# Kernel tuning notes

Measured on AMD Instinct MI355X. Metric: run time of the kernel, lower is better.

Reference implementation:

```python
import jax, jax.numpy as jnp
import numpy as np

N_NODES = 100000
N_EDGES = 1200000
D = 64  # in = hid = out = 64


def _seg_sum(vals, idx, n):
    return jax.ops.segment_sum(vals, idx, num_segments=n)


def _graph_conv(x, src, dst, W, b, n_nodes):
    # dgl.nn.GraphConv with norm='both', bias=True:
    #   h = (D_out^-1/2 applied to src feats) -> sum over edges -> D_in^-1/2 -> +b
    # Weight applied first (math-equivalent linear, in==out dims here).
    e = src.shape[0]
    ones = jnp.ones((e,), x.dtype)
    deg_out = jnp.clip(_seg_sum(ones, src, n_nodes), 1.0)  # zero-deg clamp, as in DGL
    deg_in = jnp.clip(_seg_sum(ones, dst, n_nodes), 1.0)
    h = (x @ W) * jax.lax.rsqrt(deg_out)[:, None]          # [N, D]
    agg = _seg_sum(h[src], dst, n_nodes)                   # gather-scatter over edges
    return agg * jax.lax.rsqrt(deg_in)[:, None] + b


def _rgcn(x, edges, params, n_nodes):
    # HeteroGraphConv(aggregate='sum'): sum per-relation GraphConv outputs.
    (s0, d0), (s1, d1) = edges
    h = (_graph_conv(x, s0, d0, params['W1_0'], params['b1_0'], n_nodes)
         + _graph_conv(x, s1, d1, params['W1_1'], params['b1_1'], n_nodes))
    h = jax.nn.relu(h)
    h = (_graph_conv(h, s0, d0, params['W2_0'], params['b2_0'], n_nodes)
         + _graph_conv(h, s1, d1, params['W2_1'], params['b2_1'], n_nodes))
    return h


def setup_inputs() -> dict:
    key = jax.random.key(0)
    ks = jax.random.split(key, 16)
    inp = {
        'x': jax.random.normal(ks[0], (N_NODES, D), dtype=jnp.float32),
        'rel0_src': jax.random.randint(ks[1], (N_EDGES,), 0, N_NODES, dtype=jnp.int32),
        'rel0_dst': jax.random.randint(ks[2], (N_EDGES,), 0, N_NODES, dtype=jnp.int32),
        'rel1_src': jax.random.randint(ks[3], (N_EDGES,), 0, N_NODES, dtype=jnp.int32),
        'rel1_dst': jax.random.randint(ks[4], (N_EDGES,), 0, N_NODES, dtype=jnp.int32),
        'neg_src': jax.random.randint(ks[5], (N_EDGES,), 0, N_NODES, dtype=jnp.int32),
        'neg_dst': jax.random.randint(ks[6], (N_EDGES,), 0, N_NODES, dtype=jnp.int32),
    }
    scale = 1.0 / np.sqrt(D)
    for i, name in enumerate(['W1_0', 'W1_1', 'W2_0', 'W2_1']):
        inp[name] = jax.random.normal(ks[7 + i], (D, D), dtype=jnp.float32) * scale
    for name in ['b1_0', 'b1_1', 'b2_0', 'b2_1']:
        inp[name] = jnp.zeros((D,), dtype=jnp.float32)
    return inp


def reference(x, rel0_src, rel0_dst, rel1_src, rel1_dst, neg_src, neg_dst,
              W1_0, W1_1, W2_0, W2_1, b1_0, b1_1, b2_0, b2_1):
    params = {'W1_0': W1_0, 'b1_0': b1_0, 'W1_1': W1_1, 'b1_1': b1_1,
              'W2_0': W2_0, 'b2_0': b2_0, 'W2_1': W2_1, 'b2_1': b2_1}
    edges = ((rel0_src, rel0_dst), (rel1_src, rel1_dst))
    h = _rgcn(x, edges, params, N_NODES)  # [N, D]
    # HeteroDotProductPredictor: u_dot_v on etype edges -> [E, 1]
    pos_score = jnp.sum(h[rel0_src] * h[rel0_dst], axis=-1, keepdims=True)
    neg_score = jnp.sum(h[neg_src] * h[neg_dst], axis=-1, keepdims=True)
    return pos_score, neg_score
```

## Files before the change

kernel.cpp:

```cpp
#include <hip/hip_runtime.h>
#include <hip/hip_fp16.h>

#define N_NODES 100000
#define N_EDGES 1200000
#define TOTAL_E (2 * N_EDGES)
#define D 64

#define BSH 7
#define NBUCK 782
#define NCHUNK 320
#define CHUNK 7500
#define HIST_L (NBUCK * NCHUNK)
#define SCAN_BS 256
#define SCAN_NB ((HIST_L + SCAN_BS - 1) / SCAN_BS)
#define ENT_CAP 4608
#define L2M_GRID ((N_NODES + 127) / 128)
#define NKEY 2048

typedef __attribute__((ext_vector_type(8))) short bf16x8;
typedef __attribute__((ext_vector_type(4))) float f32x4;

__device__ __forceinline__ unsigned short f32_bf16_rne(float f) {
    unsigned u = __float_as_uint(f);
    unsigned r = u + 0x7FFF + ((u >> 16) & 1);
    return (unsigned short)(r >> 16);
}
__device__ __forceinline__ float bf16_f32(unsigned short h) {
    return __uint_as_float(((unsigned)h) << 16);
}

__global__ __launch_bounds__(512) void countA_kernel(const int* __restrict__ s0,
                                                     const int* __restrict__ d0,
                                                     const int* __restrict__ s1,
                                                     const int* __restrict__ d1,
                                                     int* __restrict__ hist) {
    __shared__ int hD[NBUCK];
    __shared__ int hS[NBUCK];
    int t = threadIdx.x;
    for (int i = t; i < NBUCK; i += 512) { hD[i] = 0; hS[i] = 0; }
    __syncthreads();
    int base = blockIdx.x * CHUNK;
    for (int i = t; i < CHUNK; i += 512) {
        int e = base + i;
        int rel = (e >= N_EDGES);
        int src = rel ? s1[e - N_EDGES] : s0[e];
        int dst = rel ? d1[e - N_EDGES] : d0[e];
        atomicAdd(&hD[dst >> BSH], 1);
        atomicAdd(&hS[src >> BSH], 1);
    }
    __syncthreads();
    for (int i = t; i < NBUCK; i += 512) {
        hist[i * NCHUNK + blockIdx.x] = hD[i];
        hist[HIST_L + i * NCHUNK + blockIdx.x] = hS[i];
    }
}

__global__ void scan1_kernel(const int* __restrict__ in, int* __restrict__ out,
                             int* __restrict__ bsum) {
    __shared__ int s[SCAN_BS];
    int t = threadIdx.x;
    int i = blockIdx.x * SCAN_BS + t;
    int v = (i < HIST_L) ? in[i] : 0;
    s[t] = v;
    __syncthreads();
    for (int off = 1; off < SCAN_BS; off <<= 1) {
        int add = (t >= off) ? s[t - off] : 0;
        __syncthreads();
        s[t] += add;
        __syncthreads();
    }
    if (i < HIST_L) out[i] = s[t] - v;
    if (t == SCAN_BS - 1) bsum[blockIdx.x] = s[t];
}

__global__ void scan2_kernel(int* __restrict__ bsum) {
    __shared__ int s[1024];
    int t = threadIdx.x;
    int v = (t < SCAN_NB) ? bsum[t] : 0;
    s[t] = v;
    __syncthreads();
    for (int off = 1; off < 1024; off <<= 1) {
        int add = (t >= off) ? s[t - off] : 0;
        __syncthreads();
        s[t] += add;
        __syncthreads();
    }
    if (t < SCAN_NB) bsum[t] = s[t] - v;
}

__global__ void scan3_kernel(int* __restrict__ out, const int* __restrict__ bsum) {
    int i = blockIdx.x * SCAN_BS + threadIdx.x;
    if (i < HIST_L) out[i] += bsum[blockIdx.x];
    if (i == 0) out[HIST_L] = TOTAL_E;
}

__global__ __launch_bounds__(512) void scatterA_kernel(const int* __restrict__ s0,
                                                       const int* __restrict__ d0,
                                                       const int* __restrict__ s1,
                                                       const int* __restrict__ d1,
                                                       const int* __restrict__ ofs,
                                                       const int* __restrict__ ofsS,
                                                       unsigned* __restrict__ binned,
                                                       unsigned char* __restrict__ binnedS) {
    __shared__ int cur[NBUCK];
    __shared__ int curS[NBUCK];
    int t = threadIdx.x, wg = blockIdx.x;
    for (int b = t; b < NBUCK; b += 512) {
        cur[b] = ofs[b * NCHUNK + wg];
        curS[b] = ofsS[b * NCHUNK + wg];
    }
    __syncthreads();
    int base = wg * CHUNK;
    for (int i = t; i < CHUNK; i += 512) {
        int e = base + i;
        int rel = (e >= N_EDGES);
        int src = rel ? s1[e - N_EDGES] : s0[e];
        int dst = rel ? d1[e - N_EDGES] : d0[e];
        int p = atomicAdd(&cur[dst >> BSH], 1);
        binned[p] = (unsigned)src | ((unsigned)(dst & 127) << 17) | ((unsigned)rel << 24);
        int q = atomicAdd(&curS[src >> BSH], 1);
        binnedS[q] = (unsigned char)((src & 127) | (rel << 7));
    }
}

__global__ __launch_bounds__(512) void sortB_kernel(unsigned* __restrict__ binned,
                                                    const int* __restrict__ ofs,
                                                    int* __restrict__ ip0,
                                                    int* __restrict__ ip1,
                                                    unsigned short* __restrict__ c0a,
                                                    unsigned short* __restrict__ c1a) {
    __shared__ unsigned ent[ENT_CAP];
    __shared__ int cnt[NKEY], pfx[NKEY], cur[NKEY];
    __shared__ int tsum[512];
    int t = threadIdx.x;
    int b = blockIdx.x;
    int start = ofs[b * NCHUNK];
    int end = ofs[(b + 1) * NCHUNK];
    int n = end - start;

    for (int i = t; i < NKEY; i += 512) cnt[i] = 0;
    __syncthreads();
    for (int i = t; i < n; i += 512) {
        unsigned u = binned[start + i];
        if (i < ENT_CAP) ent[i] = u;
        int key = ((int)((u >> 17) & 255) << 3) | (int)((u & 0x1FFFFu) >> 14);
        atomicAdd(&cnt[key], 1);
    }
    __syncthreads();
    int b4 = t * 4;
    int k0 = cnt[b4], k1 = cnt[b4 + 1], k2 = cnt[b4 + 2], k3 = cnt[b4 + 3];
    int s1 = k0 + k1, s2 = s1 + k2, s3 = s2 + k3;
    tsum[t] = s3;
    __syncthreads();
    for (int off = 1; off < 512; off <<= 1) {
        int add = (t >= off) ? tsum[t - off] : 0;
        __syncthreads();
        tsum[t] += add;
        __syncthreads();
    }
    int ex = tsum[t] - s3;
    pfx[b4] = ex;
    pfx[b4 + 1] = ex + k0;
    pfx[b4 + 2] = ex + s1;
    pfx[b4 + 3] = ex + s2;
    cur[b4] = ex;
    cur[b4 + 1] = ex + k0;
    cur[b4 + 2] = ex + s1;
    cur[b4 + 3] = ex + s2;
    __syncthreads();
    for (int i = t; i < n; i += 512) {
        if (i < ENT_CAP) {
            unsigned u = ent[i];
            int key = ((int)((u >> 17) & 255) << 3) | (int)((u & 0x1FFFFu) >> 14);
            int p = atomicAdd(&cur[key], 1);
            binned[start + p] = u & 0x1FFFF;
        }
    }
    if (t < 128) {
        int node = b * 128 + t;
        if (node < N_NODES) {
            int kr0 = t << 3;
            int kr1 = (1 << 10) | (t << 3);
            int p0 = pfx[kr0];
            int e0 = pfx[kr0 + 8];
            int p1 = pfx[kr1];
            int e1 = (t == 127) ? n : pfx[kr1 + 8];
            ip0[node] = start + p0;
            ip1[node] = start + p1;
            c0a[node] = (unsigned short)(e0 - p0);
            c1a[node] = (unsigned short)(e1 - p1);
        }
    }
}

__global__ __launch_bounds__(512) void countO_kernel(const unsigned char* __restrict__ binnedS,
                                                     const int* __restrict__ ofsS,
                                                     int* __restrict__ cntO0,
                                                     int* __restrict__ cntO1) {
    __shared__ int cnt[256];
    int t = threadIdx.x;
    int b = blockIdx.x;
    int start = ofsS[b * NCHUNK];
    int end = ofsS[(b + 1) * NCHUNK];
    if (t < 256) cnt[t] = 0;
    __syncthreads();
    for (int i = start + t; i < end; i += 512)
        atomicAdd(&cnt[(int)binnedS[i]], 1);
    __syncthreads();
    if (t < 128) {
        int node = b * 128 + t;
        if (node < N_NODES) {
            cntO0[node] = cnt[t];
            cntO1[node] = cnt[t | 128];
        }
    }
}

__global__ void wprep_kernel(const float* __restrict__ W0,
                             const float* __restrict__ W1,
                             short* __restrict__ Wf) {
    int t = blockIdx.x * blockDim.x + threadIdx.x;
    if (t >= 2 * 4096) return;
    int rel = t >> 12;
    int e = t & 4095;
    int k = e >> 6, col = e & 63;
    float wv = (rel ? W1 : W0)[e];
    unsigned short hi = f32_bf16_rne(wv);
    unsigned short lo = f32_bf16_rne(wv - bf16_f32(hi));
    int kstep = k >> 5, g = (k >> 3) & 3, j = k & 7;
    int base = ((((rel * 2 + 0) * 2 + kstep) * 4 + g) * 64 + col) * 8 + j;
    int baseL = ((((rel * 2 + 1) * 2 + kstep) * 4 + g) * 64 + col) * 8 + j;
    Wf[base] = (short)hi;
    Wf[baseL] = (short)lo;
}

__global__ __launch_bounds__(256) void lin2m_kernel(const float* __restrict__ x,
                                                    const short* __restrict__ Wf,
                                                    const int* __restrict__ cntO0,
                                                    const int* __restrict__ cntO1,
                                                    __half* __restrict__ y0,
                                                    __half* __restrict__ y1) {
    int t = threadIdx.x;
    int w = t >> 6, lane = t & 63;
    int lr = lane & 15, g = lane >> 4;
    int rowbase = blockIdx.x * 128 + w * 32;

    bf16x8 ah[2][2], al[2][2];
#pragma unroll
    for (int m = 0; m < 2; ++m) {
        int row = rowbase + m * 16 + lr;
        bool ok = row < N_NODES;
        const float* xp = x + (size_t)row * 64 + g * 8;
#pragma unroll
        for (int s = 0; s < 2; ++s) {
            float fv[8];
            if (ok) {
                float4 f0 = ((const float4*)(xp + s * 32))[0];
                float4 f1 = ((const float4*)(xp + s * 32))[1];
                fv[0] = f0.x; fv[1] = f0.y; fv[2] = f0.z; fv[3] = f0.w;
                fv[4] = f1.x; fv[5] = f1.y; fv[6] = f1.z; fv[7] = f1.w;
            } else {
#pragma unroll
                for (int j = 0; j < 8; ++j) fv[j] = 0.f;
            }
#pragma unroll
            for (int j = 0; j < 8; ++j) {
                unsigned short hi = f32_bf16_rne(fv[j]);
                unsigned short lo = f32_bf16_rne(fv[j] - bf16_f32(hi));
                ah[m][s][j] = (short)hi;
                al[m][s][j] = (short)lo;
            }
        }
    }

    float rsc[2][2][4];
#pragma unroll
    for (int m = 0; m < 2; ++m)
#pragma unroll
        for (int reg = 0; reg < 4; ++reg) {
            int row = rowbase + m * 16 + g * 4 + reg;
            bool ok = row < N_NODES;
            rsc[0][m][reg] = ok ? rsqrtf((float)max(cntO0[row], 1)) : 1.f;
            rsc[1][m][reg] = ok ? rsqrtf((float)max(cntO1[row], 1)) : 1.f;
        }

#pragma unroll
    for (int rel = 0; rel < 2; ++rel) {
        __half* yo = rel ? y1 : y0;
        const short* wr = Wf + rel * 8192 + g * 512;
#pragma unroll
        for (int n = 0; n < 4; ++n) {
            const short* wb = wr + (n * 16 + lr) * 8;
            bf16x8 wh0 = *(const bf16x8*)(wb);
            bf16x8 wh1 = *(const bf16x8*)(wb + 2048);
            bf16x8 wl0 = *(const bf16x8*)(wb + 4096);
            bf16x8 wl1 = *(const bf16x8*)(wb + 6144);
#pragma unroll
            for (int m = 0; m < 2; ++m) {
                f32x4 acc = {0.f, 0.f, 0.f, 0.f};
                acc = __builtin_amdgcn_mfma_f32_16x16x32_bf16(al[m][0], wh0, acc, 0, 0, 0);
                acc = __builtin_amdgcn_mfma_f32_16x16x32_bf16(ah[m][0], wl0, acc, 0, 0, 0);
                acc = __builtin_amdgcn_mfma_f32_16x16x32_bf16(ah[m][0], wh0, acc, 0, 0, 0);
                acc = __builtin_amdgcn_mfma_f32_16x16x32_bf16(al[m][1], wh1, acc, 0, 0, 0);
                acc = __builtin_amdgcn_mfma_f32_16x16x32_bf16(ah[m][1], wl1, acc, 0, 0, 0);
                acc = __builtin_amdgcn_mfma_f32_16x16x32_bf16(ah[m][1], wh1, acc, 0, 0, 0);
#pragma unroll
                for (int reg = 0; reg < 4; ++reg) {
                    int row = rowbase + m * 16 + g * 4 + reg;
                    if (row < N_NODES)
                        yo[(size_t)row * 64 + n * 16 + lr] =
                            __float2half_rn(acc[reg] * rsc[rel][m][reg]);
                }
            }
        }
    }
}

template <int RELU, int OUTH>
__global__ __launch_bounds__(256) void aggC_kernel(const __half* __restrict__ L0,
                                                   const __half* __restrict__ L1,
                                                   const unsigned* __restrict__ es,
                                                   const int* __restrict__ ip0,
                                                   const int* __restrict__ ip1,
                                                   const unsigned short* __restrict__ c0a,
                                                   const unsigned short* __restrict__ c1a,
                                                   const float* __restrict__ bia0,
                                                   const float* __restrict__ bia1,
                                                   float* __restrict__ outf,
                                                   __half* __restrict__ outh) {
    int t = threadIdx.x;
    int g = t >> 3, l8 = t & 7;
    int node = blockIdx.x * 32 + g;
    if (node >= N_NODES) return;

    int st0 = ip0[node], c0 = c0a[node];
    int st1 = ip1[node], c1 = c1a[node];

    float a[8] = {0, 0, 0, 0, 0, 0, 0, 0};
    float b[8] = {0, 0, 0, 0, 0, 0, 0, 0};
    union HU { uint4 u; __half2 h[4]; };

    for (int k = 0; k < c0; ++k) {
        int s = (int)es[st0 + k];
        HU uu;
        uu.u = ((const uint4*)(L0 + (size_t)s * 64))[l8];
#pragma unroll
        for (int q = 0; q < 4; ++q) {
            float2 f = __half22float2(uu.h[q]);
            a[2 * q] += f.x;
            a[2 * q + 1] += f.y;
        }
    }
    for (int k = 0; k < c1; ++k) {
        int s = (int)es[st1 + k];
        HU uu;
        uu.u = ((const uint4*)(L1 + (size_t)s * 64))[l8];
#pragma unroll
        for (int q = 0; q < 4; ++q) {
            float2 f = __half22float2(uu.h[q]);
            b[2 * q] += f.x;
            b[2 * q + 1] += f.y;
        }
    }

    float r0 = rsqrtf((float)max(c0, 1));
    float r1 = rsqrtf((float)max(c1, 1));
    float4 u0a = ((const float4*)bia0)[l8 * 2];
    float4 u0b = ((const float4*)bia0)[l8 * 2 + 1];
    float4 u1a = ((const float4*)bia1)[l8 * 2];
    float4 u1b = ((const float4*)bia1)[l8 * 2 + 1];
    float o[8];
#pragma unroll
    for (int q = 0; q < 8; ++q) o[q] = a[q] * r0 + b[q] * r1;
    o[0] += u0a.x + u1a.x; o[1] += u0a.y + u1a.y;
    o[2] += u0a.z + u1a.z; o[3] += u0a.w + u1a.w;
    o[4] += u0b.x + u1b.x; o[5] += u0b.y + u1b.y;
    o[6] += u0b.z + u1b.z; o[7] += u0b.w + u1b.w;
    if (RELU) {
#pragma unroll
        for (int q = 0; q < 8; ++q) o[q] = fmaxf(o[q], 0.f);
    }
    if (OUTH) {
        HU vv;
#pragma unroll
        for (int q = 0; q < 4; ++q)
            vv.h[q] = __floats2half2_rn(o[2 * q], o[2 * q + 1]);
        ((uint4*)(outh + (size_t)node * 64))[l8] = vv.u;
    } else {
        float4 f0 = {o[0], o[1], o[2], o[3]};
        float4 f1 = {o[4], o[5], o[6], o[7]};
        ((float4*)(outf + (size_t)node * 64))[l8 * 2] = f0;
        ((float4*)(outf + (size_t)node * 64))[l8 * 2 + 1] = f1;
    }
}

__global__ __launch_bounds__(256) void score_kernel(const __half* __restrict__ h2,
                                                    const int* __restrict__ ps,
                                                    const int* __restrict__ pd,
                                                    const int* __restrict__ ns,
                                                    const int* __restrict__ nd,
                                                    float* __restrict__ out) {
    int gid = blockIdx.x * blockDim.x + threadIdx.x;
    int e = gid >> 3;
    int l8 = gid & 7;
    if (e >= 2 * N_EDGES) return;
    int s, d;
    if (e < N_EDGES) { s = ps[e]; d = pd[e]; }
    else             { s = ns[e - N_EDGES]; d = nd[e - N_EDGES]; }
    union HU { uint4 u; __half2 h[4]; };
    HU ua, ub;
    ua.u = ((const uint4*)(h2 + (size_t)s * 64))[l8];
    ub.u = ((const uint4*)(h2 + (size_t)d * 64))[l8];
    float p = 0.f;
#pragma unroll
    for (int q = 0; q < 4; ++q) {
        float2 fa = __half22float2(ua.h[q]);
        float2 fb = __half22float2(ub.h[q]);
        p += fa.x * fb.x + fa.y * fb.y;
    }
    p += __shfl_xor(p, 1);
    p += __shfl_xor(p, 2);
    p += __shfl_xor(p, 4);
    if (l8 == 0) out[e] = p;
}

extern "C" void kernel_launch(void* const* d_in, const int* in_sizes, int n_in,
                              void* d_out, int out_size, void* d_ws, size_t ws_size,
                              hipStream_t stream) {
    const float* x    = (const float*)d_in[0];
    const int* s0     = (const int*)d_in[1];
    const int* d0     = (const int*)d_in[2];
    const int* s1     = (const int*)d_in[3];
    const int* d1     = (const int*)d_in[4];
    const int* nsrc   = (const int*)d_in[5];
    const int* ndst   = (const int*)d_in[6];
    const float* W1_0 = (const float*)d_in[7];
    const float* W1_1 = (const float*)d_in[8];
    const float* W2_0 = (const float*)d_in[9];
    const float* W2_1 = (const float*)d_in[10];
    const float* b1_0 = (const float*)d_in[11];
    const float* b1_1 = (const float*)d_in[12];
    const float* b2_0 = (const float*)d_in[13];
    const float* b2_1 = (const float*)d_in[14];
    float* out = (float*)d_out;

    char* p = (char*)d_ws;
    int* cntO0 = (int*)p;      p += N_NODES * 4;
    int* cntO1 = (int*)p;      p += N_NODES * 4;
    int* hist  = (int*)p;      p += 2 * HIST_L * 4;
    int* ofs   = (int*)p;      p += (HIST_L + 1) * 4;
    int* ofsS  = (int*)p;      p += (HIST_L + 1) * 4;
    int* bsum  = (int*)p;      p += 1024 * 4;
    unsigned* binned = (unsigned*)p;  p += (size_t)TOTAL_E * 4;
    int* ip0   = (int*)p;      p += N_NODES * 4;
    int* ip1   = (int*)p;      p += N_NODES * 4;
    unsigned short* c0a = (unsigned short*)p;  p += N_NODES * 2;
    unsigned short* c1a = (unsigned short*)p;  p += N_NODES * 2;
    unsigned char* binnedS = (unsigned char*)p;  p += (size_t)TOTAL_E;
    p = (char*)(((size_t)p + 255) & ~(size_t)255);
    short* WfA = (short*)p;    p += 16384 * 2;
    short* WfB = (short*)p;    p += 16384 * 2;
    p = (char*)(((size_t)p + 255) & ~(size_t)255);
    __half* bufL0h = (__half*)p;  p += (size_t)N_NODES * D * 2;
    __half* bufL1h = (__half*)p;  p += (size_t)N_NODES * D * 2;
    __half* h2h    = (__half*)p;  p += (size_t)N_NODES * D * 2;
    p = (char*)(((size_t)p + 255) & ~(size_t)255);
    float* bufH = (float*)p;   p += (size_t)N_NODES * D * 4;

    const int aggGrid  = (N_NODES + 31) / 32;
    const int scorGrid = (2 * N_EDGES * 8) / 256;

    wprep_kernel<<<32, 256, 0, stream>>>(W1_0, W1_1, WfA);
    wprep_kernel<<<32, 256, 0, stream>>>(W2_0, W2_1, WfB);

    countA_kernel<<<NCHUNK, 512, 0, stream>>>(s0, d0, s1, d1, hist);
    scan1_kernel<<<SCAN_NB, SCAN_BS, 0, stream>>>(hist, ofs, bsum);
    scan2_kernel<<<1, 1024, 0, stream>>>(bsum);
    scan3_kernel<<<SCAN_NB, SCAN_BS, 0, stream>>>(ofs, bsum);
    scan1_kernel<<<SCAN_NB, SCAN_BS, 0, stream>>>(hist + HIST_L, ofsS, bsum);
    scan2_kernel<<<1, 1024, 0, stream>>>(bsum);
    scan3_kernel<<<SCAN_NB, SCAN_BS, 0, stream>>>(ofsS, bsum);
    scatterA_kernel<<<NCHUNK, 512, 0, stream>>>(s0, d0, s1, d1, ofs, ofsS, binned, binnedS);
    sortB_kernel<<<NBUCK, 512, 0, stream>>>(binned, ofs, ip0, ip1, c0a, c1a);
    countO_kernel<<<NBUCK, 512, 0, stream>>>(binnedS, ofsS, cntO0, cntO1);

    lin2m_kernel<<<L2M_GRID, 256, 0, stream>>>(x, WfA, cntO0, cntO1, bufL0h, bufL1h);
    aggC_kernel<1, 0><<<aggGrid, 256, 0, stream>>>(bufL0h, bufL1h, binned, ip0, ip1,
                                                   c0a, c1a, b1_0, b1_1, bufH, nullptr);

    lin2m_kernel<<<L2M_GRID, 256, 0, stream>>>(bufH, WfB, cntO0, cntO1, bufL0h, bufL1h);
    aggC_kernel<0, 1><<<aggGrid, 256, 0, stream>>>(bufL0h, bufL1h, binned, ip0, ip1,
                                                   c0a, c1a, b2_0, b2_1, nullptr, h2h);

    score_kernel<<<scorGrid, 256, 0, stream>>>(h2h, s0, d0, nsrc, ndst, out);
}
```

Measured before the change: 340.5 us.

## Merge dual prefix scans, unroll aggregation gathers by two, score two edges per thread

The two histogram prefix scans (dst and src buckets) are merged into a single scan over the concatenated array, dropping three kernel launches. Source offsets are recovered by subtracting TOTAL_E, and scan2 now handles two block sums per thread. The aggregation loop is unrolled by two with separate accumulators so more independent gathers are in flight. The score kernel processes two edges per lane group and writes a float2, which halves the grid but raises register use per thread.

```diff
diff --git a/kernel.cpp b/kernel.cpp
--- a/kernel.cpp
+++ b/kernel.cpp
@@ -11,8 +11,9 @@
 #define NCHUNK 320
 #define CHUNK 7500
 #define HIST_L (NBUCK * NCHUNK)
+#define HIST2 (2 * HIST_L)
 #define SCAN_BS 256
-#define SCAN_NB ((HIST_L + SCAN_BS - 1) / SCAN_BS)
+#define SCAN_NB2 ((HIST2 + SCAN_BS - 1) / SCAN_BS)
 #define ENT_CAP 4608
 #define L2M_GRID ((N_NODES + 127) / 128)
 #define NKEY 2048
@@ -60,7 +61,7 @@
     __shared__ int s[SCAN_BS];
     int t = threadIdx.x;
     int i = blockIdx.x * SCAN_BS + t;
-    int v = (i < HIST_L) ? in[i] : 0;
+    int v = (i < HIST2) ? in[i] : 0;
     s[t] = v;
     __syncthreads();
     for (int off = 1; off < SCAN_BS; off <<= 1) {
@@ -69,15 +70,17 @@
         s[t] += add;
         __syncthreads();
     }
-    if (i < HIST_L) out[i] = s[t] - v;
+    if (i < HIST2) out[i] = s[t] - v;
     if (t == SCAN_BS - 1) bsum[blockIdx.x] = s[t];
 }
 
 __global__ void scan2_kernel(int* __restrict__ bsum) {
     __shared__ int s[1024];
     int t = threadIdx.x;
-    int v = (t < SCAN_NB) ? bsum[t] : 0;
-    s[t] = v;
+    int v0 = (2 * t < SCAN_NB2) ? bsum[2 * t] : 0;
+    int v1 = (2 * t + 1 < SCAN_NB2) ? bsum[2 * t + 1] : 0;
+    int sum = v0 + v1;
+    s[t] = sum;
     __syncthreads();
     for (int off = 1; off < 1024; off <<= 1) {
         int add = (t >= off) ? s[t - off] : 0;
@@ -85,29 +88,30 @@
         s[t] += add;
         __syncthreads();
     }
-    if (t < SCAN_NB) bsum[t] = s[t] - v;
+    int ex = s[t] - sum;
+    if (2 * t < SCAN_NB2) bsum[2 * t] = ex;
+    if (2 * t + 1 < SCAN_NB2) bsum[2 * t + 1] = ex + v0;
 }
 
 __global__ void scan3_kernel(int* __restrict__ out, const int* __restrict__ bsum) {
     int i = blockIdx.x * SCAN_BS + threadIdx.x;
-    if (i < HIST_L) out[i] += bsum[blockIdx.x];
-    if (i == 0) out[HIST_L] = TOTAL_E;
+    if (i < HIST2) out[i] += bsum[blockIdx.x];
+    if (i == 0) out[HIST2] = 2 * TOTAL_E;
 }
 
 __global__ __launch_bounds__(512) void scatterA_kernel(const int* __restrict__ s0,
                                                        const int* __restrict__ d0,
                                                        const int* __restrict__ s1,
                                                        const int* __restrict__ d1,
-                                                       const int* __restrict__ ofs,
-                                                       const int* __restrict__ ofsS,
+                                                       const int* __restrict__ OFS,
                                                        unsigned* __restrict__ binned,
                                                        unsigned char* __restrict__ binnedS) {
     __shared__ int cur[NBUCK];
     __shared__ int curS[NBUCK];
     int t = threadIdx.x, wg = blockIdx.x;
     for (int b = t; b < NBUCK; b += 512) {
-        cur[b] = ofs[b * NCHUNK + wg];
-        curS[b] = ofsS[b * NCHUNK + wg];
+        cur[b] = OFS[b * NCHUNK + wg];
+        curS[b] = OFS[HIST_L + b * NCHUNK + wg] - TOTAL_E;
     }
     __syncthreads();
     int base = wg * CHUNK;
@@ -124,7 +128,7 @@
 }
 
 __global__ __launch_bounds__(512) void sortB_kernel(unsigned* __restrict__ binned,
-                                                    const int* __restrict__ ofs,
+                                                    const int* __restrict__ OFS,
                                                     int* __restrict__ ip0,
                                                     int* __restrict__ ip1,
                                                     unsigned short* __restrict__ c0a,
@@ -134,8 +138,8 @@
     __shared__ int tsum[512];
     int t = threadIdx.x;
     int b = blockIdx.x;
-    int start = ofs[b * NCHUNK];
-    int end = ofs[(b + 1) * NCHUNK];
+    int start = OFS[b * NCHUNK];
+    int end = OFS[(b + 1) * NCHUNK];
     int n = end - start;
 
     for (int i = t; i < NKEY; i += 512) cnt[i] = 0;
@@ -194,14 +198,14 @@
 }
 
 __global__ __launch_bounds__(512) void countO_kernel(const unsigned char* __restrict__ binnedS,
-                                                     const int* __restrict__ ofsS,
+                                                     const int* __restrict__ OFS,
                                                      int* __restrict__ cntO0,
                                                      int* __restrict__ cntO1) {
     __shared__ int cnt[256];
     int t = threadIdx.x;
     int b = blockIdx.x;
-    int start = ofsS[b * NCHUNK];
-    int end = ofsS[(b + 1) * NCHUNK];
+    int start = OFS[HIST_L + b * NCHUNK] - TOTAL_E;
+    int end = OFS[HIST_L + (b + 1) * NCHUNK] - TOTAL_E;
     if (t < 256) cnt[t] = 0;
     __syncthreads();
     for (int i = start + t; i < end; i += 512)
@@ -337,10 +341,27 @@
     int st1 = ip1[node], c1 = c1a[node];
 
     float a[8] = {0, 0, 0, 0, 0, 0, 0, 0};
+    float a2[8] = {0, 0, 0, 0, 0, 0, 0, 0};
     float b[8] = {0, 0, 0, 0, 0, 0, 0, 0};
+    float b2[8] = {0, 0, 0, 0, 0, 0, 0, 0};
     union HU { uint4 u; __half2 h[4]; };
 
-    for (int k = 0; k < c0; ++k) {
+    int k = 0;
+    for (; k + 2 <= c0; k += 2) {
+        int sA = (int)es[st0 + k];
+        int sB = (int)es[st0 + k + 1];
+        HU uA, uB;
+        uA.u = ((const uint4*)(L0 + (size_t)sA * 64))[l8];
+        uB.u = ((const uint4*)(L0 + (size_t)sB * 64))[l8];
+#pragma unroll
+        for (int q = 0; q < 4; ++q) {
+            float2 fA = __half22float2(uA.h[q]);
+            float2 fB = __half22float2(uB.h[q]);
+            a[2 * q] += fA.x;  a[2 * q + 1] += fA.y;
+            a2[2 * q] += fB.x; a2[2 * q + 1] += fB.y;
+        }
+    }
+    if (k < c0) {
         int s = (int)es[st0 + k];
         HU uu;
         uu.u = ((const uint4*)(L0 + (size_t)s * 64))[l8];
@@ -351,7 +372,22 @@
             a[2 * q + 1] += f.y;
         }
     }
-    for (int k = 0; k < c1; ++k) {
+    k = 0;
+    for (; k + 2 <= c1; k += 2) {
+        int sA = (int)es[st1 + k];
+        int sB = (int)es[st1 + k + 1];
+        HU uA, uB;
+        uA.u = ((const uint4*)(L1 + (size_t)sA * 64))[l8];
+        uB.u = ((const uint4*)(L1 + (size_t)sB * 64))[l8];
+#pragma unroll
+        for (int q = 0; q < 4; ++q) {
+            float2 fA = __half22float2(uA.h[q]);
+            float2 fB = __half22float2(uB.h[q]);
+            b[2 * q] += fA.x;  b[2 * q + 1] += fA.y;
+            b2[2 * q] += fB.x; b2[2 * q + 1] += fB.y;
+        }
+    }
+    if (k < c1) {
         int s = (int)es[st1 + k];
         HU uu;
         uu.u = ((const uint4*)(L1 + (size_t)s * 64))[l8];
@@ -371,7 +407,7 @@
     float4 u1b = ((const float4*)bia1)[l8 * 2 + 1];
     float o[8];
 #pragma unroll
-    for (int q = 0; q < 8; ++q) o[q] = a[q] * r0 + b[q] * r1;
+    for (int q = 0; q < 8; ++q) o[q] = (a[q] + a2[q]) * r0 + (b[q] + b2[q]) * r1;
     o[0] += u0a.x + u1a.x; o[1] += u0a.y + u1a.y;
     o[2] += u0a.z + u1a.z; o[3] += u0a.w + u1a.w;
     o[4] += u0b.x + u1b.x; o[5] += u0b.y + u1b.y;
@@ -401,27 +437,40 @@
                                                     const int* __restrict__ nd,
                                                     float* __restrict__ out) {
     int gid = blockIdx.x * blockDim.x + threadIdx.x;
-    int e = gid >> 3;
+    int pr = gid >> 3;
     int l8 = gid & 7;
-    if (e >= 2 * N_EDGES) return;
-    int s, d;
-    if (e < N_EDGES) { s = ps[e]; d = pd[e]; }
-    else             { s = ns[e - N_EDGES]; d = nd[e - N_EDGES]; }
+    int e0 = pr * 2;
+    if (e0 >= TOTAL_E) return;
+    int e1 = e0 + 1;
+    int sA, dA, sB, dB;
+    if (e0 < N_EDGES) { sA = ps[e0]; dA = pd[e0]; sB = ps[e1]; dB = pd[e1]; }
+    else {
+        sA = ns[e0 - N_EDGES]; dA = nd[e0 - N_EDGES];
+        sB = ns[e1 - N_EDGES]; dB = nd[e1 - N_EDGES];
+    }
     union HU { uint4 u; __half2 h[4]; };
-    HU ua, ub;
-    ua.u = ((const uint4*)(h2 + (size_t)s * 64))[l8];
-    ub.u = ((const uint4*)(h2 + (size_t)d * 64))[l8];
-    float p = 0.f;
+    HU ua0, ub0, ua1, ub1;
+    ua0.u = ((const uint4*)(h2 + (size_t)sA * 64))[l8];
+    ub0.u = ((const uint4*)(h2 + (size_t)dA * 64))[l8];
+    ua1.u = ((const uint4*)(h2 + (size_t)sB * 64))[l8];
+    ub1.u = ((const uint4*)(h2 + (size_t)dB * 64))[l8];
+    float p0 = 0.f, p1 = 0.f;
 #pragma unroll
     for (int q = 0; q < 4; ++q) {
-        float2 fa = __half22float2(ua.h[q]);
-        float2 fb = __half22float2(ub.h[q]);
-        p += fa.x * fb.x + fa.y * fb.y;
-    }
-    p += __shfl_xor(p, 1);
-    p += __shfl_xor(p, 2);
-    p += __shfl_xor(p, 4);
-    if (l8 == 0) out[e] = p;
+        float2 fa0 = __half22float2(ua0.h[q]);
+        float2 fb0 = __half22float2(ub0.h[q]);
+        float2 fa1 = __half22float2(ua1.h[q]);
+        float2 fb1 = __half22float2(ub1.h[q]);
+        p0 += fa0.x * fb0.x + fa0.y * fb0.y;
+        p1 += fa1.x * fb1.x + fa1.y * fb1.y;
+    }
+    p0 += __shfl_xor(p0, 1);
+    p0 += __shfl_xor(p0, 2);
+    p0 += __shfl_xor(p0, 4);
+    p1 += __shfl_xor(p1, 1);
+    p1 += __shfl_xor(p1, 2);
+    p1 += __shfl_xor(p1, 4);
+    if (l8 == 0) ((float2*)out)[pr] = make_float2(p0, p1);
 }
 
 extern "C" void kernel_launch(void* const* d_in, const int* in_sizes, int n_in,
@@ -447,10 +496,9 @@
     char* p = (char*)d_ws;
     int* cntO0 = (int*)p;      p += N_NODES * 4;
     int* cntO1 = (int*)p;      p += N_NODES * 4;
-    int* hist  = (int*)p;      p += 2 * HIST_L * 4;
-    int* ofs   = (int*)p;      p += (HIST_L + 1) * 4;
-    int* ofsS  = (int*)p;      p += (HIST_L + 1) * 4;
-    int* bsum  = (int*)p;      p += 1024 * 4;
+    int* hist  = (int*)p;      p += (size_t)HIST2 * 4;
+    int* OFS   = (int*)p;      p += ((size_t)HIST2 + 8) * 4;
+    int* bsum  = (int*)p;      p += 2048 * 4;
     unsigned* binned = (unsigned*)p;  p += (size_t)TOTAL_E * 4;
     int* ip0   = (int*)p;      p += N_NODES * 4;
     int* ip1   = (int*)p;      p += N_NODES * 4;
@@ -468,21 +516,18 @@
     float* bufH = (float*)p;   p += (size_t)N_NODES * D * 4;
 
     const int aggGrid  = (N_NODES + 31) / 32;
-    const int scorGrid = (2 * N_EDGES * 8) / 256;
+    const int scorGrid = (TOTAL_E / 2 * 8 + 255) / 256;
 
     wprep_kernel<<<32, 256, 0, stream>>>(W1_0, W1_1, WfA);
     wprep_kernel<<<32, 256, 0, stream>>>(W2_0, W2_1, WfB);
 
     countA_kernel<<<NCHUNK, 512, 0, stream>>>(s0, d0, s1, d1, hist);
-    scan1_kernel<<<SCAN_NB, SCAN_BS, 0, stream>>>(hist, ofs, bsum);
+    scan1_kernel<<<SCAN_NB2, SCAN_BS, 0, stream>>>(hist, OFS, bsum);
     scan2_kernel<<<1, 1024, 0, stream>>>(bsum);
-    scan3_kernel<<<SCAN_NB, SCAN_BS, 0, stream>>>(ofs, bsum);
-    scan1_kernel<<<SCAN_NB, SCAN_BS, 0, stream>>>(hist + HIST_L, ofsS, bsum);
-    scan2_kernel<<<1, 1024, 0, stream>>>(bsum);
-    scan3_kernel<<<SCAN_NB, SCAN_BS, 0, stream>>>(ofsS, bsum);
-    scatterA_kernel<<<NCHUNK, 512, 0, stream>>>(s0, d0, s1, d1, ofs, ofsS, binned, binnedS);
-    sortB_kernel<<<NBUCK, 512, 0, stream>>>(binned, ofs, ip0, ip1, c0a, c1a);
-    countO_kernel<<<NBUCK, 512, 0, stream>>>(binnedS, ofsS, cntO0, cntO1);
+    scan3_kernel<<<SCAN_NB2, SCAN_BS, 0, stream>>>(OFS, bsum);
+    scatterA_kernel<<<NCHUNK, 512, 0, stream>>>(s0, d0, s1, d1, OFS, binned, binnedS);
+    sortB_kernel<<<NBUCK, 512, 0, stream>>>(binned, OFS, ip0, ip1, c0a, c1a);
+    countO_kernel<<<NBUCK, 512, 0, stream>>>(binnedS, OFS, cntO0, cntO1);
 
     lin2m_kernel<<<L2M_GRID, 256, 0, stream>>>(x, WfA, cntO0, cntO1, bufL0h, bufL1h);
     aggC_kernel<1, 0><<<aggGrid, 256, 0, stream>>>(bufL0h, bufL1h, binned, ip0, ip1,
```

Result: faster. 299.9 us (-11.9%).
